# Optimization experiments

Hardware: AMD Instinct MI355X
Metric: run time of the kernel (lower is better)

Reference implementation:

```python
import jax, jax.numpy as jnp
import numpy as np

B, S, D, H, HD, F = 8, 1024, 512, 8, 64, 2048
EPS = 1e-6

def rmsnorm(x, w):
    var = jnp.mean(x * x, axis=-1, keepdims=True)
    return w * (x * jax.lax.rsqrt(var + EPS))

def setup_inputs() -> dict:
    key = jax.random.key(0)
    ks = jax.random.split(key, 10)
    sd = 512 ** -0.5
    return {
        "primals_1": jax.random.normal(ks[0], (D, D), jnp.float32) * sd,
        "primals_2": jax.random.normal(ks[1], (D, D), jnp.float32) * sd,
        "primals_3": jax.random.normal(ks[2], (D, D), jnp.float32) * sd,
        "primals_4": jax.random.normal(ks[3], (D, D), jnp.float32) * sd,
        "primals_5": jax.random.uniform(ks[4], (D,), jnp.float32, 0.5, 1.5),
        "primals_6": jax.random.normal(ks[5], (F, D), jnp.float32) * sd,
        "primals_7": jax.random.normal(ks[6], (D, F), jnp.float32) * (F ** -0.5),
        "primals_8": jax.random.uniform(ks[7], (D,), jnp.float32, 0.5, 1.5),
        "primals_9": jax.random.normal(ks[8], (B, S, D), jnp.float32),
        "primals_10": jax.random.normal(ks[9], (B, H, S, S), jnp.float32) * 0.1,
    }

def reference(primals_1, primals_2, primals_3, primals_4, primals_5,
              primals_6, primals_7, primals_8, primals_9, primals_10):
    x = primals_9
    # --- self-attention sublayer ---
    h = rmsnorm(x, primals_5)                      # [B,S,D]
    # T5: no 1/sqrt(head_dim) scaling
    q = (h @ primals_3.T).reshape(B, S, H, HD).transpose(0, 2, 1, 3)  # [B,H,S,HD]
    k = (h @ primals_1.T).reshape(B, S, H, HD).transpose(0, 2, 1, 3)
    v = (h @ primals_4.T).reshape(B, S, H, HD).transpose(0, 2, 1, 3)
    scores = jnp.einsum('bhqd,bhkd->bhqk', q, k) + primals_10        # [B,H,S,S]
    attn = jax.nn.softmax(scores, axis=-1)
    ctx = jnp.einsum('bhqk,bhkd->bhqd', attn, v)                     # [B,H,S,HD]
    ctx = ctx.transpose(0, 2, 1, 3).reshape(B, S, D)
    x = x + ctx @ primals_2.T                       # residual add_1
    # --- FFN sublayer ---
    h2 = rmsnorm(x, primals_8)
    ff = jax.nn.relu(h2 @ primals_6.T)              # [B,S,F]
    out = x + ff @ primals_7.T                      # add_3
    return out
```

## Files before the change

kernel.cpp:

```cpp
#include <hip/hip_runtime.h>

#define B_ 8
#define S_ 1024
#define D_ 512
#define H_ 8
#define HD_ 64
#define F_ 2048

typedef unsigned short u16;
typedef __attribute__((ext_vector_type(8))) short bf16x8;
typedef __attribute__((ext_vector_type(4))) float f32x4;

__device__ __forceinline__ float bf2f(u16 u) {
  union { unsigned int i; float f; } v; v.i = ((unsigned int)u) << 16; return v.f;
}
__device__ __forceinline__ u16 f2bf(float f) {
  union { float f; unsigned int i; } v; v.f = f;
  unsigned int r = v.i + 0x7fffu + ((v.i >> 16) & 1u);
  return (u16)(r >> 16);
}

__device__ __forceinline__ void gl2lds16(const u16* g, u16* lds) {
  __builtin_amdgcn_global_load_lds(
      (const __attribute__((address_space(1))) unsigned int*)g,
      (__attribute__((address_space(3))) unsigned int*)lds, 16, 0, 0);
}

__global__ __launch_bounds__(256) void cvt_w_k(const float* __restrict__ wq, const float* __restrict__ wk,
                                               const float* __restrict__ wv, const float* __restrict__ wo,
                                               const float* __restrict__ wf1, const float* __restrict__ wf2,
                                               u16* __restrict__ dst) {
  size_t gid = (size_t)blockIdx.x * 256 + threadIdx.x;
  size_t e0 = gid * 4;
  const float* src; size_t loc;
  if      (e0 <  262144) { src = wq;  loc = e0; }
  else if (e0 <  524288) { src = wk;  loc = e0 -  262144; }
  else if (e0 <  786432) { src = wv;  loc = e0 -  524288; }
  else if (e0 < 1048576) { src = wo;  loc = e0 -  786432; }
  else if (e0 < 2097152) { src = wf1; loc = e0 - 1048576; }
  else                   { src = wf2; loc = e0 - 2097152; }
  float4 v = *(const float4*)(src + loc);
  ushort4 o; o.x = f2bf(v.x); o.y = f2bf(v.y); o.z = f2bf(v.z); o.w = f2bf(v.w);
  *(ushort4*)(dst + e0) = o;
}

template <int IN_BF16>
__global__ __launch_bounds__(256) void rmsnorm_k(const void* __restrict__ xv,
                                                 const float* __restrict__ w,
                                                 u16* __restrict__ out) {
  int row = blockIdx.x;
  int tid = threadIdx.x;
  float x0, x1;
  if (IN_BF16) {
    const u16* xr = (const u16*)xv + (size_t)row * D_;
    x0 = bf2f(xr[tid]); x1 = bf2f(xr[tid + 256]);
  } else {
    const float* xr = (const float*)xv + (size_t)row * D_;
    x0 = xr[tid]; x1 = xr[tid + 256];
  }
  float s = x0 * x0 + x1 * x1;
#pragma unroll
  for (int off = 32; off >= 1; off >>= 1) s += __shfl_xor(s, off, 64);
  __shared__ float red[4];
  int lane = tid & 63, wid = tid >> 6;
  if (lane == 0) red[wid] = s;
  __syncthreads();
  float tot = red[0] + red[1] + red[2] + red[3];
  float inv = rsqrtf(tot * (1.0f / D_) + 1e-6f);
  u16* orow = out + (size_t)row * D_;
  orow[tid]       = f2bf(x0 * inv * w[tid]);
  orow[tid + 256] = f2bf(x1 * inv * w[tid + 256]);
}

template <int RELU, int RMODE, int OF32>
__global__ __launch_bounds__(256) void gemm_mfma_k(const u16* __restrict__ A,
                                                   const u16* __restrict__ W,
                                                   const void* __restrict__ Rv,
                                                   void* __restrict__ Cv,
                                                   int M, int N, int K) {
  __shared__ __align__(16) u16 As[128 * 32];
  __shared__ __align__(16) u16 Bs[128 * 32];
  int tid = threadIdx.x;
  int w = tid >> 6, l = tid & 63;
  int quad = l >> 4, l16 = l & 15;
  int m0 = blockIdx.y * 128, n0 = blockIdx.x * 128;
  int wr = (w >> 1) * 64, wc = (w & 1) * 64;

  int c_sw = (l & 3) ^ ((l >> 2) & 3);
  int r_in = l >> 2;
  int swz = quad ^ (l16 & 3);

  f32x4 acc[4][4];
#pragma unroll
  for (int i = 0; i < 4; i++)
#pragma unroll
    for (int j = 0; j < 4; j++) acc[i][j] = (f32x4)(0.0f);

  for (int k0 = 0; k0 < K; k0 += 32) {
    __syncthreads();
#pragma unroll
    for (int t = 0; t < 2; t++) {
      int chunk = w * 2 + t;
      int row = chunk * 16 + r_in;
      gl2lds16(A + (size_t)(m0 + row) * K + k0 + c_sw * 8, As + chunk * 512);
      gl2lds16(W + (size_t)(n0 + row) * K + k0 + c_sw * 8, Bs + chunk * 512);
    }
    __syncthreads();
    bf16x8 af[4], bf[4];
#pragma unroll
    for (int i = 0; i < 4; i++)
      af[i] = *(const bf16x8*)(As + (wr + i * 16 + l16) * 32 + swz * 8);
#pragma unroll
    for (int j = 0; j < 4; j++)
      bf[j] = *(const bf16x8*)(Bs + (wc + j * 16 + l16) * 32 + swz * 8);
#pragma unroll
    for (int i = 0; i < 4; i++)
#pragma unroll
      for (int j = 0; j < 4; j++)
        acc[i][j] = __builtin_amdgcn_mfma_f32_16x16x32_bf16(af[i], bf[j], acc[i][j], 0, 0, 0);
  }

#pragma unroll
  for (int i = 0; i < 4; i++)
#pragma unroll
    for (int r = 0; r < 4; r++) {
      int mrow = m0 + wr + i * 16 + quad * 4 + r;
      size_t base = (size_t)mrow * N + n0 + wc + l16;
#pragma unroll
      for (int j = 0; j < 4; j++) {
        float v = acc[i][j][r];
        if (RELU) v = fmaxf(v, 0.0f);
        if (RMODE == 1) v += ((const float*)Rv)[base + j * 16];
        if (RMODE == 2) v += bf2f(((const u16*)Rv)[base + j * 16]);
        if (OF32) ((float*)Cv)[base + j * 16] = v;
        else      ((u16*)Cv)[base + j * 16]   = f2bf(v);
      }
    }
}

__global__ __launch_bounds__(256) void transpose_v_k(const u16* __restrict__ qkv,
                                                     u16* __restrict__ vt) {
  __shared__ u16 T[64][72];
  int t = threadIdx.x;
  int s0 = blockIdx.x * 64, h = blockIdx.y, b = blockIdx.z;
  int skey = t >> 3, dch = (t & 7) * 8;
#pragma unroll
  for (int rnd = 0; rnd < 2; rnd++) {
    int s = s0 + skey + rnd * 32;
    bf16x8 vv = *(const bf16x8*)(qkv + ((size_t)(b * S_) + s) * 1536 + 1024 + h * HD_ + dch);
#pragma unroll
    for (int i = 0; i < 8; i++) T[dch + i][skey + rnd * 32] = (u16)((short*)&vv)[i];
  }
  __syncthreads();
  int d = t >> 2, kc = (t & 3) * 16;
  bf16x8 a0 = *(const bf16x8*)(&T[d][kc]);
  bf16x8 a1 = *(const bf16x8*)(&T[d][kc + 8]);
  u16* dst = vt + ((size_t)(b * H_ + h) * HD_ + d) * S_ + s0 + kc;
  *(bf16x8*)dst       = a0;
  *(bf16x8*)(dst + 8) = a1;
}

__global__ __launch_bounds__(256) void attn_v2_k(const u16* __restrict__ qkv,
                                                 const u16* __restrict__ vt,
                                                 const float* __restrict__ bias,
                                                 u16* __restrict__ ctx) {
  int tid = threadIdx.x;
  int w = tid >> 6, lane = tid & 63;
  int quad = lane >> 4, l16 = lane & 15;
  int h = blockIdx.y, b = blockIdx.z;
  int q0 = blockIdx.x * 64;

  __shared__ __align__(16) u16 KsA[64 * 32];
  __shared__ __align__(16) u16 KsB[64 * 32];
  __shared__ __align__(16) u16 VsA[64 * 32];
  __shared__ __align__(16) u16 VsB[64 * 32];
  __shared__ __align__(16) u16 Pl[4][16 * 72];

  const u16* qrow = qkv + ((size_t)(b * S_) + q0 + w * 16 + l16) * 1536 + h * HD_;
  bf16x8 qf0 = *(const bf16x8*)(qrow + quad * 8);
  bf16x8 qf1 = *(const bf16x8*)(qrow + 32 + quad * 8);

  float mr[4], lr[4];
  f32x4 Oacc[4];
#pragma unroll
  for (int r = 0; r < 4; r++) { mr[r] = -1e30f; lr[r] = 0.0f; }
#pragma unroll
  for (int nt = 0; nt < 4; nt++) Oacc[nt] = (f32x4)(0.0f);

  const float* bpw = bias + ((size_t)((b * H_ + h) * S_) + q0 + w * 16) * S_;

  int srow = w * 16 + (lane >> 2);
  int sc   = lane & 3;
  int slc  = sc ^ (srow & 3);
  u16* ldsKA = KsA + w * 512;
  u16* ldsKB = KsB + w * 512;
  u16* ldsVA = VsA + w * 512;
  u16* ldsVB = VsB + w * 512;

  for (int kt = 0; kt < S_; kt += 64) {
    __syncthreads();
    {
      const u16* krow = qkv + ((size_t)(b * S_) + kt + srow) * 1536 + 512 + h * HD_;
      gl2lds16(krow + slc * 8, ldsKA);
      gl2lds16(krow + 32 + slc * 8, ldsKB);
      const u16* vrow = vt + ((size_t)(b * H_ + h) * HD_ + srow) * S_ + kt;
      gl2lds16(vrow + slc * 8, ldsVA);
      gl2lds16(vrow + 32 + slc * 8, ldsVB);
    }
    __syncthreads();

    f32x4 sg[4];
#pragma unroll
    for (int g = 0; g < 4; g++) {
      int row = g * 16 + l16;
      int sw = quad ^ (row & 3);
      bf16x8 kf0 = *(const bf16x8*)(KsA + row * 32 + sw * 8);
      bf16x8 kf1 = *(const bf16x8*)(KsB + row * 32 + sw * 8);
      f32x4 a = (f32x4)(0.0f);
      a = __builtin_amdgcn_mfma_f32_16x16x32_bf16(qf0, kf0, a, 0, 0, 0);
      a = __builtin_amdgcn_mfma_f32_16x16x32_bf16(qf1, kf1, a, 0, 0, 0);
      sg[g] = a;
    }
#pragma unroll
    for (int r = 0; r < 4; r++) {
      size_t bro = (size_t)(quad * 4 + r) * S_ + kt + l16;
      float b0 = bpw[bro];
      float b1 = bpw[bro + 16];
      float b2 = bpw[bro + 32];
      float b3 = bpw[bro + 48];
      float s0 = sg[0][r] + b0, s1 = sg[1][r] + b1, s2 = sg[2][r] + b2, s3 = sg[3][r] + b3;
      float t = fmaxf(fmaxf(s0, s1), fmaxf(s2, s3));
      t = fmaxf(t, __shfl_xor(t, 1, 64));
      t = fmaxf(t, __shfl_xor(t, 2, 64));
      t = fmaxf(t, __shfl_xor(t, 4, 64));
      t = fmaxf(t, __shfl_xor(t, 8, 64));
      float mn = fmaxf(mr[r], t);
      float alpha = __expf(mr[r] - mn);
      float p0 = __expf(s0 - mn), p1 = __expf(s1 - mn);
      float p2 = __expf(s2 - mn), p3 = __expf(s3 - mn);
      float rs = (p0 + p1) + (p2 + p3);
      rs += __shfl_xor(rs, 1, 64);
      rs += __shfl_xor(rs, 2, 64);
      rs += __shfl_xor(rs, 4, 64);
      rs += __shfl_xor(rs, 8, 64);
      lr[r] = lr[r] * alpha + rs;
      mr[r] = mn;
#pragma unroll
      for (int nt = 0; nt < 4; nt++) Oacc[nt][r] *= alpha;
      u16* prow = &Pl[w][(quad * 4 + r) * 72];
      prow[l16]      = f2bf(p0);
      prow[16 + l16] = f2bf(p1);
      prow[32 + l16] = f2bf(p2);
      prow[48 + l16] = f2bf(p3);
    }
    bf16x8 pf0 = *(const bf16x8*)(&Pl[w][l16 * 72 + quad * 8]);
    bf16x8 pf1 = *(const bf16x8*)(&Pl[w][l16 * 72 + 32 + quad * 8]);
#pragma unroll
    for (int nt = 0; nt < 4; nt++) {
      int row = nt * 16 + l16;
      int sw = quad ^ (row & 3);
      bf16x8 vf0 = *(const bf16x8*)(VsA + row * 32 + sw * 8);
      bf16x8 vf1 = *(const bf16x8*)(VsB + row * 32 + sw * 8);
      Oacc[nt] = __builtin_amdgcn_mfma_f32_16x16x32_bf16(pf0, vf0, Oacc[nt], 0, 0, 0);
      Oacc[nt] = __builtin_amdgcn_mfma_f32_16x16x32_bf16(pf1, vf1, Oacc[nt], 0, 0, 0);
    }
  }

  size_t obase = ((size_t)(b * S_) + q0 + w * 16) * D_ + h * HD_;
#pragma unroll
  for (int r = 0; r < 4; r++) {
    float inv = 1.0f / lr[r];
    int qr = quad * 4 + r;
#pragma unroll
    for (int nt = 0; nt < 4; nt++) {
      ctx[obase + (size_t)qr * D_ + nt * 16 + l16] = f2bf(Oacc[nt][r] * inv);
    }
  }
}

extern "C" void kernel_launch(void* const* d_in, const int* in_sizes, int n_in,
                              void* d_out, int out_size, void* d_ws, size_t ws_size,
                              hipStream_t stream) {
  const float* Wk   = (const float*)d_in[0];
  const float* Wo   = (const float*)d_in[1];
  const float* Wq   = (const float*)d_in[2];
  const float* Wv   = (const float*)d_in[3];
  const float* g1   = (const float*)d_in[4];
  const float* Wf1  = (const float*)d_in[5];
  const float* Wf2  = (const float*)d_in[6];
  const float* g2   = (const float*)d_in[7];
  const float* X    = (const float*)d_in[8];
  const float* bias = (const float*)d_in[9];
  float* out = (float*)d_out;

  const size_t MD = (size_t)B_ * S_ * D_;
  u16* wbf   = (u16*)d_ws;
  u16* Wqkvb = wbf;
  u16* Wob   = wbf +  786432;
  u16* Wf1b  = wbf + 1048576;
  u16* Wf2b  = wbf + 2097152;
  u16* h     = wbf + 3145728;
  u16* qkv   = h + MD;
  u16* vtb   = qkv + 3 * MD;
  u16* ctx   = vtb + MD;
  u16* ff    = ctx + MD;
  u16* x1    = qkv;
  u16* h2    = h;

  dim3 blk(256);
  const int M = B_ * S_;

  cvt_w_k<<<3072, blk, 0, stream>>>(Wq, Wk, Wv, Wo, Wf1, Wf2, wbf);

  rmsnorm_k<0><<<M, blk, 0, stream>>>(X, g1, h);

  dim3 gqkv(1536 / 128, M / 128);
  gemm_mfma_k<0, 0, 0><<<gqkv, blk, 0, stream>>>(h, Wqkvb, nullptr, qkv, M, 1536, D_);

  dim3 gt(S_ / 64, H_, B_);
  transpose_v_k<<<gt, blk, 0, stream>>>(qkv, vtb);

  dim3 ga(S_ / 64, H_, B_);
  attn_v2_k<<<ga, blk, 0, stream>>>(qkv, vtb, bias, ctx);

  dim3 g512(D_ / 128, M / 128);
  gemm_mfma_k<0, 1, 0><<<g512, blk, 0, stream>>>(ctx, Wob, X, x1, M, D_, D_);

  rmsnorm_k<1><<<M, blk, 0, stream>>>(x1, g2, h2);

  dim3 gff1(F_ / 128, M / 128);
  gemm_mfma_k<1, 0, 0><<<gff1, blk, 0, stream>>>(h2, Wf1b, nullptr, ff, M, F_, D_);

  gemm_mfma_k<0, 2, 1><<<g512, blk, 0, stream>>>(ff, Wf2b, x1, out, M, D_, F_);
}
```

Before: 578.7 us.

## Retile N=512 GEMMs, load attention K/V directly, vectorize rmsnorm and transpose stores

```diff
diff --git a/kernel.cpp b/kernel.cpp
--- a/kernel.cpp
+++ b/kernel.cpp
@@ -8,6 +8,7 @@
 #define F_ 2048
 
 typedef unsigned short u16;
+typedef unsigned int u32;
 typedef __attribute__((ext_vector_type(8))) short bf16x8;
 typedef __attribute__((ext_vector_type(4))) float f32x4;
 
@@ -52,11 +53,11 @@
   int tid = threadIdx.x;
   float x0, x1;
   if (IN_BF16) {
-    const u16* xr = (const u16*)xv + (size_t)row * D_;
-    x0 = bf2f(xr[tid]); x1 = bf2f(xr[tid + 256]);
+    u32 v = ((const u32*)((const u16*)xv + (size_t)row * D_))[tid];
+    x0 = bf2f((u16)(v & 0xffffu)); x1 = bf2f((u16)(v >> 16));
   } else {
-    const float* xr = (const float*)xv + (size_t)row * D_;
-    x0 = xr[tid]; x1 = xr[tid + 256];
+    float2 v = ((const float2*)((const float*)xv + (size_t)row * D_))[tid];
+    x0 = v.x; x1 = v.y;
   }
   float s = x0 * x0 + x1 * x1;
 #pragma unroll
@@ -67,61 +68,64 @@
   __syncthreads();
   float tot = red[0] + red[1] + red[2] + red[3];
   float inv = rsqrtf(tot * (1.0f / D_) + 1e-6f);
-  u16* orow = out + (size_t)row * D_;
-  orow[tid]       = f2bf(x0 * inv * w[tid]);
-  orow[tid + 256] = f2bf(x1 * inv * w[tid + 256]);
-}
-
-template <int RELU, int RMODE, int OF32>
+  float2 wv = ((const float2*)w)[tid];
+  u32 o = (u32)f2bf(x0 * inv * wv.x) | ((u32)f2bf(x1 * inv * wv.y) << 16);
+  ((u32*)(out + (size_t)row * D_))[tid] = o;
+}
+
+template <int RELU, int RMODE, int OF32, int BM>
 __global__ __launch_bounds__(256) void gemm_mfma_k(const u16* __restrict__ A,
                                                    const u16* __restrict__ W,
                                                    const void* __restrict__ Rv,
                                                    void* __restrict__ Cv,
                                                    int M, int N, int K) {
-  __shared__ __align__(16) u16 As[128 * 32];
+  constexpr int MI  = BM / 32;
+  constexpr int ACH = BM / 16;
+  __shared__ __align__(16) u16 As[BM * 32];
   __shared__ __align__(16) u16 Bs[128 * 32];
   int tid = threadIdx.x;
   int w = tid >> 6, l = tid & 63;
   int quad = l >> 4, l16 = l & 15;
-  int m0 = blockIdx.y * 128, n0 = blockIdx.x * 128;
-  int wr = (w >> 1) * 64, wc = (w & 1) * 64;
+  int m0 = blockIdx.y * BM, n0 = blockIdx.x * 128;
+  int wr = (w >> 1) * (BM / 2), wc = (w & 1) * 64;
 
   int c_sw = (l & 3) ^ ((l >> 2) & 3);
   int r_in = l >> 2;
   int swz = quad ^ (l16 & 3);
 
-  f32x4 acc[4][4];
-#pragma unroll
-  for (int i = 0; i < 4; i++)
+  f32x4 acc[MI][4];
+#pragma unroll
+  for (int i = 0; i < MI; i++)
 #pragma unroll
     for (int j = 0; j < 4; j++) acc[i][j] = (f32x4)(0.0f);
 
   for (int k0 = 0; k0 < K; k0 += 32) {
     __syncthreads();
 #pragma unroll
-    for (int t = 0; t < 2; t++) {
-      int chunk = w * 2 + t;
-      int row = chunk * 16 + r_in;
-      gl2lds16(A + (size_t)(m0 + row) * K + k0 + c_sw * 8, As + chunk * 512);
-      gl2lds16(W + (size_t)(n0 + row) * K + k0 + c_sw * 8, Bs + chunk * 512);
+    for (int t = 0; t < (ACH + 8) / 4; t++) {
+      int ch = w * ((ACH + 8) / 4) + t;
+      const u16* src; u16* dst;
+      if (ch < ACH) { src = A + (size_t)(m0 + ch * 16 + r_in) * K;        dst = As + ch * 512; }
+      else          { src = W + (size_t)(n0 + (ch - ACH) * 16 + r_in) * K; dst = Bs + (ch - ACH) * 512; }
+      gl2lds16(src + k0 + c_sw * 8, dst);
     }
     __syncthreads();
-    bf16x8 af[4], bf[4];
-#pragma unroll
-    for (int i = 0; i < 4; i++)
+    bf16x8 af[MI], bf[4];
+#pragma unroll
+    for (int i = 0; i < MI; i++)
       af[i] = *(const bf16x8*)(As + (wr + i * 16 + l16) * 32 + swz * 8);
 #pragma unroll
     for (int j = 0; j < 4; j++)
       bf[j] = *(const bf16x8*)(Bs + (wc + j * 16 + l16) * 32 + swz * 8);
 #pragma unroll
-    for (int i = 0; i < 4; i++)
+    for (int i = 0; i < MI; i++)
 #pragma unroll
       for (int j = 0; j < 4; j++)
         acc[i][j] = __builtin_amdgcn_mfma_f32_16x16x32_bf16(af[i], bf[j], acc[i][j], 0, 0, 0);
   }
 
 #pragma unroll
-  for (int i = 0; i < 4; i++)
+  for (int i = 0; i < MI; i++)
 #pragma unroll
     for (int r = 0; r < 4; r++) {
       int mrow = m0 + wr + i * 16 + quad * 4 + r;
@@ -144,12 +148,16 @@
   int t = threadIdx.x;
   int s0 = blockIdx.x * 64, h = blockIdx.y, b = blockIdx.z;
   int skey = t >> 3, dch = (t & 7) * 8;
+  int rot = dch >> 3;
 #pragma unroll
   for (int rnd = 0; rnd < 2; rnd++) {
     int s = s0 + skey + rnd * 32;
     bf16x8 vv = *(const bf16x8*)(qkv + ((size_t)(b * S_) + s) * 1536 + 1024 + h * HD_ + dch);
 #pragma unroll
-    for (int i = 0; i < 8; i++) T[dch + i][skey + rnd * 32] = (u16)((short*)&vv)[i];
+    for (int i = 0; i < 8; i++) {
+      int ii = (i + rot) & 7;
+      T[dch + ii][skey + rnd * 32] = (u16)((short*)&vv)[ii];
+    }
   }
   __syncthreads();
   int d = t >> 2, kc = (t & 3) * 16;
@@ -160,7 +168,7 @@
   *(bf16x8*)(dst + 8) = a1;
 }
 
-__global__ __launch_bounds__(256) void attn_v2_k(const u16* __restrict__ qkv,
+__global__ __launch_bounds__(256) void attn_v3_k(const u16* __restrict__ qkv,
                                                  const u16* __restrict__ vt,
                                                  const float* __restrict__ bias,
                                                  u16* __restrict__ ctx) {
@@ -170,10 +178,6 @@
   int h = blockIdx.y, b = blockIdx.z;
   int q0 = blockIdx.x * 64;
 
-  __shared__ __align__(16) u16 KsA[64 * 32];
-  __shared__ __align__(16) u16 KsB[64 * 32];
-  __shared__ __align__(16) u16 VsA[64 * 32];
-  __shared__ __align__(16) u16 VsB[64 * 32];
   __shared__ __align__(16) u16 Pl[4][16 * 72];
 
   const u16* qrow = qkv + ((size_t)(b * S_) + q0 + w * 16 + l16) * 1536 + h * HD_;
@@ -188,39 +192,23 @@
   for (int nt = 0; nt < 4; nt++) Oacc[nt] = (f32x4)(0.0f);
 
   const float* bpw = bias + ((size_t)((b * H_ + h) * S_) + q0 + w * 16) * S_;
-
-  int srow = w * 16 + (lane >> 2);
-  int sc   = lane & 3;
-  int slc  = sc ^ (srow & 3);
-  u16* ldsKA = KsA + w * 512;
-  u16* ldsKB = KsB + w * 512;
-  u16* ldsVA = VsA + w * 512;
-  u16* ldsVB = VsB + w * 512;
+  const u16* kbase = qkv + (size_t)(b * S_) * 1536 + 512 + h * HD_ + quad * 8;
+  const u16* vbase = vt + (size_t)((b * H_ + h) * HD_) * S_ + quad * 8;
 
   for (int kt = 0; kt < S_; kt += 64) {
-    __syncthreads();
-    {
-      const u16* krow = qkv + ((size_t)(b * S_) + kt + srow) * 1536 + 512 + h * HD_;
-      gl2lds16(krow + slc * 8, ldsKA);
-      gl2lds16(krow + 32 + slc * 8, ldsKB);
-      const u16* vrow = vt + ((size_t)(b * H_ + h) * HD_ + srow) * S_ + kt;
-      gl2lds16(vrow + slc * 8, ldsVA);
-      gl2lds16(vrow + 32 + slc * 8, ldsVB);
-    }
-    __syncthreads();
-
     f32x4 sg[4];
+    __builtin_amdgcn_s_setprio(1);
 #pragma unroll
     for (int g = 0; g < 4; g++) {
-      int row = g * 16 + l16;
-      int sw = quad ^ (row & 3);
-      bf16x8 kf0 = *(const bf16x8*)(KsA + row * 32 + sw * 8);
-      bf16x8 kf1 = *(const bf16x8*)(KsB + row * 32 + sw * 8);
+      const u16* kp = kbase + (size_t)(kt + g * 16 + l16) * 1536;
+      bf16x8 kf0 = *(const bf16x8*)kp;
+      bf16x8 kf1 = *(const bf16x8*)(kp + 32);
       f32x4 a = (f32x4)(0.0f);
       a = __builtin_amdgcn_mfma_f32_16x16x32_bf16(qf0, kf0, a, 0, 0, 0);
       a = __builtin_amdgcn_mfma_f32_16x16x32_bf16(qf1, kf1, a, 0, 0, 0);
       sg[g] = a;
     }
+    __builtin_amdgcn_s_setprio(0);
 #pragma unroll
     for (int r = 0; r < 4; r++) {
       size_t bro = (size_t)(quad * 4 + r) * S_ + kt + l16;
@@ -255,15 +243,16 @@
     }
     bf16x8 pf0 = *(const bf16x8*)(&Pl[w][l16 * 72 + quad * 8]);
     bf16x8 pf1 = *(const bf16x8*)(&Pl[w][l16 * 72 + 32 + quad * 8]);
+    __builtin_amdgcn_s_setprio(1);
 #pragma unroll
     for (int nt = 0; nt < 4; nt++) {
-      int row = nt * 16 + l16;
-      int sw = quad ^ (row & 3);
-      bf16x8 vf0 = *(const bf16x8*)(VsA + row * 32 + sw * 8);
-      bf16x8 vf1 = *(const bf16x8*)(VsB + row * 32 + sw * 8);
+      const u16* vp = vbase + (size_t)(nt * 16 + l16) * S_ + kt;
+      bf16x8 vf0 = *(const bf16x8*)vp;
+      bf16x8 vf1 = *(const bf16x8*)(vp + 32);
       Oacc[nt] = __builtin_amdgcn_mfma_f32_16x16x32_bf16(pf0, vf0, Oacc[nt], 0, 0, 0);
       Oacc[nt] = __builtin_amdgcn_mfma_f32_16x16x32_bf16(pf1, vf1, Oacc[nt], 0, 0, 0);
     }
+    __builtin_amdgcn_s_setprio(0);
   }
 
   size_t obase = ((size_t)(b * S_) + q0 + w * 16) * D_ + h * HD_;
@@ -315,21 +304,21 @@
   rmsnorm_k<0><<<M, blk, 0, stream>>>(X, g1, h);
 
   dim3 gqkv(1536 / 128, M / 128);
-  gemm_mfma_k<0, 0, 0><<<gqkv, blk, 0, stream>>>(h, Wqkvb, nullptr, qkv, M, 1536, D_);
+  gemm_mfma_k<0, 0, 0, 128><<<gqkv, blk, 0, stream>>>(h, Wqkvb, nullptr, qkv, M, 1536, D_);
 
   dim3 gt(S_ / 64, H_, B_);
   transpose_v_k<<<gt, blk, 0, stream>>>(qkv, vtb);
 
   dim3 ga(S_ / 64, H_, B_);
-  attn_v2_k<<<ga, blk, 0, stream>>>(qkv, vtb, bias, ctx);
-
-  dim3 g512(D_ / 128, M / 128);
-  gemm_mfma_k<0, 1, 0><<<g512, blk, 0, stream>>>(ctx, Wob, X, x1, M, D_, D_);
+  attn_v3_k<<<ga, blk, 0, stream>>>(qkv, vtb, bias, ctx);
+
+  dim3 g512b(D_ / 128, M / 64);
+  gemm_mfma_k<0, 1, 0, 64><<<g512b, blk, 0, stream>>>(ctx, Wob, X, x1, M, D_, D_);
 
   rmsnorm_k<1><<<M, blk, 0, stream>>>(x1, g2, h2);
 
   dim3 gff1(F_ / 128, M / 128);
-  gemm_mfma_k<1, 0, 0><<<gff1, blk, 0, stream>>>(h2, Wf1b, nullptr, ff, M, F_, D_);
-
-  gemm_mfma_k<0, 2, 1><<<g512, blk, 0, stream>>>(ff, Wf2b, x1, out, M, D_, F_);
-}
+  gemm_mfma_k<1, 0, 0, 128><<<gff1, blk, 0, stream>>>(h2, Wf1b, nullptr, ff, M, F_, D_);
+
+  gemm_mfma_k<0, 2, 1, 64><<<g512b, blk, 0, stream>>>(ff, Wf2b, x1, out, M, D_, F_);
+}
```

After: 644.9 us. +11.4%, slower.
